# Performance work log

Hardware: AMD Instinct MI355X
Metric: run time of the kernel (lower is better)

Reference implementation:

```python
import jax, jax.numpy as jnp
import numpy as np

B, N, NODE_DIM = 64, 64, 192
H = 256          # node_hidden_dim
PDIM = 64        # property_embedding_dim
NUM_EDGE_TYPE = 5
T = 4            # message-passing rounds
E = 16384        # total edges (flattened batched graph)
E_SEL = 65536    # selected candidate pairs


def setup_inputs() -> dict:
    key = jax.random.key(0)
    ks = jax.random.split(key, 24)
    def g(k, shape, scale=0.05):
        return jax.random.normal(k, shape, dtype=jnp.float32) * scale
    inp = {
        "x": jax.random.normal(ks[0], (B, N, NODE_DIM), dtype=jnp.float32),
        "edge_index": jax.random.randint(ks[1], (2, E), 0, B * N, dtype=jnp.int32),
        "edge_attr": jax.random.uniform(ks[2], (E, NUM_EDGE_TYPE), dtype=jnp.float32),
        "props": jax.random.normal(ks[3], (B, 1), dtype=jnp.float32),
        "sel_b": jax.random.randint(ks[4], (E_SEL,), 0, B, dtype=jnp.int32),
        "sel_i": jax.random.randint(ks[5], (E_SEL,), 0, N, dtype=jnp.int32),
        "sel_j": jax.random.randint(ks[6], (E_SEL,), 0, N, dtype=jnp.int32),
        "golden_edge": jax.random.randint(ks[7], (E_SEL,), 0, NUM_EDGE_TYPE, dtype=jnp.int32),
        # parameters
        "W_prop": g(ks[8], (1, PDIM)), "b_prop": jnp.zeros((PDIM,), jnp.float32),
        "W_in": g(ks[9], (NODE_DIM, H)), "b_in": jnp.zeros((H,), jnp.float32),
        "W_msg": g(ks[10], (H + NUM_EDGE_TYPE, H)), "b_msg": jnp.zeros((H,), jnp.float32),
        "W_upd": g(ks[11], (2 * H, H)), "b_upd": jnp.zeros((H,), jnp.float32),
        "W_add": g(ks[12], (H + PDIM, H)), "b_add": jnp.zeros((H,), jnp.float32),
        "W1": g(ks[13], (2 * H, H)), "b1": jnp.zeros((H,), jnp.float32),
        "W2": g(ks[14], (H, H)), "b2": jnp.zeros((H,), jnp.float32),
        "W3": g(ks[15], (H, 2 * H)), "b3": jnp.zeros((2 * H,), jnp.float32),
        "W_out": g(ks[16], (2 * H, NUM_EDGE_TYPE)), "b_out": jnp.zeros((NUM_EDGE_TYPE,), jnp.float32),
    }
    return inp


def reference(x, edge_index, edge_attr, props, sel_b, sel_i, sel_j, golden_edge,
              W_prop, b_prop, W_in, b_in, W_msg, b_msg, W_upd, b_upd,
              W_add, b_add, W1, b1, W2, b2, W3, b3, W_out, b_out):
    BN = B * N
    node_x = x.reshape(BN, NODE_DIM)
    src, dst = edge_index[0], edge_index[1]

    # --- GNN node embedding (t rounds of message passing, opaque Encoder.embed_node) ---
    h = jax.nn.relu(node_x @ W_in + b_in)                       # [BN, H]
    for _ in range(T):
        msg_in = jnp.concatenate([h[src], edge_attr], axis=-1)  # [E, H+num_edge_type]
        msg = jax.nn.relu(msg_in @ W_msg + b_msg)               # [E, H]
        agg = jax.ops.segment_sum(msg, dst, num_segments=BN)    # [BN, H]
        h = jax.nn.relu(jnp.concatenate([h, agg], axis=-1) @ W_upd + b_upd)

    node_emb = h.reshape(B, N, H)

    # --- property conditioning + addition linear ---
    prop = props @ W_prop + b_prop                               # [B, PDIM]
    propp = jnp.broadcast_to(prop[:, None, :], (B, N, PDIM))
    node_embg = jnp.concatenate([node_emb, propp], axis=-1) @ W_add + b_add  # [B, N, H]

    # --- gather selected (src, dst) pairs directly (equiv. to repeat_interleave + boolean mask) ---
    flat = node_embg.reshape(BN, H)
    src_e = flat[sel_b * N + sel_i]                              # [E_SEL, H]
    dst_e = flat[sel_b * N + sel_j]                              # [E_SEL, H]
    pair = jnp.concatenate([src_e, dst_e], axis=-1)              # [E_SEL, 2H]

    # --- edge predictor MLP (3 layers, ReLU between) + output linear ---
    h1 = jax.nn.relu(pair @ W1 + b1)
    h2 = jax.nn.relu(h1 @ W2 + b2)
    h3 = h2 @ W3 + b3
    logits = h3 @ W_out + b_out                                  # [E_SEL, num_edge_type]

    # --- cross entropy (mean) ---
    logp = jax.nn.log_softmax(logits, axis=-1)
    loss = -jnp.mean(jnp.take_along_axis(logp, golden_edge[:, None].astype(jnp.int32), axis=-1))
    return loss
```

## Files before the change

### kernel.cpp

```cpp
#include <hip/hip_runtime.h>
#include <math.h>

#define BN 4096
#define N_PER_B 64
#define NE 16384
#define NSEL 65536
#define NET 5
#define PD 64
#define H1STR 260
#define FSTR 264
#define PTILES 4

typedef float f32x4 __attribute__((ext_vector_type(4)));
typedef float f32x16 __attribute__((ext_vector_type(16)));
typedef short short8 __attribute__((ext_vector_type(8)));
typedef short short4v __attribute__((ext_vector_type(4)));

__device__ __forceinline__ unsigned short f2bf(float f) {
    unsigned int u = __builtin_bit_cast(unsigned int, f);
    u += 0x7fff + ((u >> 16) & 1);
    return (unsigned short)(u >> 16);
}
__device__ __forceinline__ float bf_lo(unsigned int u) {
    return __builtin_bit_cast(float, u << 16);
}
__device__ __forceinline__ float bf_hi(unsigned int u) {
    return __builtin_bit_cast(float, u & 0xffff0000u);
}
__device__ __forceinline__ unsigned int pack2(float a, float b) {
    return (unsigned)f2bf(a) | ((unsigned)f2bf(b) << 16);
}
__device__ __forceinline__ short8 ld_frag(const unsigned short* p) {
    const short4v lo = *(const short4v*)(p);
    const short4v hi = *(const short4v*)(p + 4);
    return __builtin_shufflevector(lo, hi, 0, 1, 2, 3, 4, 5, 6, 7);
}
__device__ __forceinline__ unsigned int addrelu2(unsigned int a, unsigned int b, unsigned int c) {
    const float lo = fmaxf(bf_lo(a) + bf_lo(b) + bf_lo(c), 0.f);
    const float hi = fmaxf(bf_hi(a) + bf_hi(b) + bf_hi(c), 0.f);
    return pack2(lo, hi);
}

__global__ __launch_bounds__(256) void k_hist(const int* __restrict__ eidx,
                                              int* __restrict__ deg)
{
    const int e = blockIdx.x * 256 + threadIdx.x;
    atomicAdd(&deg[eidx[NE + e]], 1);
}

__global__ __launch_bounds__(256) void csr_scan(const int* __restrict__ deg,
                                                int* __restrict__ row_start,
                                                int* __restrict__ cursor)
{
    __shared__ int sums[256];
    const int tid = threadIdx.x;
    const int base = tid * 16;
    int local[16];
    int s = 0;
    #pragma unroll
    for (int i = 0; i < 16; ++i) { local[i] = s; s += deg[base + i]; }
    sums[tid] = s;
    __syncthreads();
    for (int off = 1; off < 256; off <<= 1) {
        const int v = sums[tid];
        const int add = (tid >= off) ? sums[tid - off] : 0;
        __syncthreads();
        sums[tid] = v + add;
        __syncthreads();
    }
    const int offset = (tid == 0) ? 0 : sums[tid - 1];
    #pragma unroll
    for (int i = 0; i < 16; ++i) {
        const int v = offset + local[i];
        row_start[base + i] = v;
        cursor[base + i] = v;
    }
    if (tid == 255) row_start[4096] = NE;
}

__global__ __launch_bounds__(256) void csr_scatter(const int* __restrict__ eidx,
                                                   int* __restrict__ cursor,
                                                   int* __restrict__ srcs,
                                                   int* __restrict__ epos)
{
    const int e = blockIdx.x * 256 + threadIdx.x;
    const int pos = atomicAdd(&cursor[eidx[NE + e]], 1);
    srcs[pos] = eidx[e];
    epos[e] = pos;
}

__global__ __launch_bounds__(256) void k_pre(
    const float* __restrict__ W_in, const float* __restrict__ W_msg,
    const float* __restrict__ W_upd, const float* __restrict__ W_add,
    const float* __restrict__ W1, const float* __restrict__ W2,
    const float* __restrict__ W3, const float* __restrict__ b3,
    const float* __restrict__ W_out, const float* __restrict__ b_out,
    const float* __restrict__ props, const float* __restrict__ W_prop,
    const float* __restrict__ b_prop, const float* __restrict__ b_add,
    const float* __restrict__ b_msg, const float* __restrict__ eattr,
    const int* __restrict__ epos,
    unsigned short* __restrict__ wbf, unsigned short* __restrict__ WfT,
    float* __restrict__ bfv, float* __restrict__ prop_add,
    unsigned short* __restrict__ ETc)
{
    __shared__ __align__(16) char smem[16704];
    const int blk = blockIdx.x;
    const int tid = threadIdx.x;

    if (blk < 128) {
        float (*s)[65] = (float(*)[65])smem;
        const int wsel = blk >> 4;
        const int sub = blk & 15;
        const float* src; unsigned short* dst; int K = 256;
        switch (wsel) {
            case 0: src = W_in;              dst = wbf;                         K = 192; break;
            case 1: src = W_msg;             dst = wbf + 49152;                 break;
            case 2: src = W_upd;             dst = wbf + 49152 + 65536;         break;
            case 3: src = W_upd + 256 * 256; dst = wbf + 49152 + 2 * 65536;     break;
            case 4: src = W_add;             dst = wbf + 49152 + 3 * 65536;     break;
            case 5: src = W1;                dst = wbf + 49152 + 4 * 65536;     break;
            case 6: src = W1 + 256 * 256;    dst = wbf + 49152 + 5 * 65536;     break;
            default: src = W2;               dst = wbf + 49152 + 6 * 65536;     break;
        }
        const int k0 = (sub >> 2) * 64;
        const int n0 = (sub & 3) * 64;
        if (k0 >= K) return;
        const int tn = tid & 63;
        const int tg = tid >> 6;
        #pragma unroll
        for (int i = 0; i < 16; ++i) {
            const int kk = tg * 16 + i;
            s[kk][tn] = src[(size_t)(k0 + kk) * 256 + n0 + tn];
        }
        __syncthreads();
        #pragma unroll
        for (int i = 0; i < 16; ++i) {
            const int nn = tg * 16 + i;
            dst[(size_t)(n0 + nn) * K + k0 + tn] = f2bf(s[tn][nn]);
        }
    } else if (blk < 192) {
        const int b = blk - 128;
        const float pv = props[b];
        float acc = b_add[tid];
        for (int p = 0; p < PD; ++p) {
            const float e = fmaf(pv, W_prop[p], b_prop[p]);
            acc = fmaf(e, W_add[(256 + p) * 256 + tid], acc);
        }
        prop_add[b * 256 + tid] = acc;
    } else if (blk < 449) {
        float* part = (float*)smem;
        const int cb = blk - 192;
        float acc[NET] = {0.f, 0.f, 0.f, 0.f, 0.f};
        #pragma unroll
        for (int rep = 0; rep < 2; ++rep) {
            const int j = rep * 256 + tid;
            const float wv = (cb < 256) ? W3[(size_t)cb * 512 + j] : b3[j];
            #pragma unroll
            for (int t = 0; t < NET; ++t) acc[t] = fmaf(wv, W_out[j * NET + t], acc[t]);
        }
        #pragma unroll
        for (int t = 0; t < NET; ++t)
            for (int off = 32; off >= 1; off >>= 1) acc[t] += __shfl_down(acc[t], off);
        if ((tid & 63) == 0) {
            #pragma unroll
            for (int t = 0; t < NET; ++t) part[(tid >> 6) * NET + t] = acc[t];
        }
        __syncthreads();
        if (tid == 0) {
            float s[NET];
            #pragma unroll
            for (int t = 0; t < NET; ++t)
                s[t] = part[t] + part[NET + t] + part[2 * NET + t] + part[3 * NET + t];
            if (cb < 256) {
                #pragma unroll
                for (int t = 0; t < NET; ++t) WfT[t * 256 + cb] = f2bf(s[t]);
                #pragma unroll
                for (int t = NET; t < 16; ++t) WfT[t * 256 + cb] = 0;
            } else {
                #pragma unroll
                for (int t = 0; t < NET; ++t) bfv[t] = s[t] + b_out[t];
            }
        }
    } else {
        float* ea = (float*)smem;
        int* eposs = (int*)(smem + 2560 + 64);
        const int eb = (blk - 449) * 128;
        if (tid < 160)
            *(float4*)&ea[tid * 4] = *(const float4*)(eattr + (size_t)eb * 5 + tid * 4);
        if (tid < 128) eposs[tid] = epos[eb + tid];
        __syncthreads();
        const float* Wme = W_msg + 256 * 256;
        const float w0 = Wme[0 * 256 + tid];
        const float w1 = Wme[1 * 256 + tid];
        const float w2 = Wme[2 * 256 + tid];
        const float w3 = Wme[3 * 256 + tid];
        const float w4 = Wme[4 * 256 + tid];
        const float bm = b_msg[tid];
        for (int i = 0; i < 128; ++i) {
            const float* a = ea + i * 5;
            float v = bm;
            v = fmaf(a[0], w0, v); v = fmaf(a[1], w1, v); v = fmaf(a[2], w2, v);
            v = fmaf(a[3], w3, v); v = fmaf(a[4], w4, v);
            ETc[(size_t)eposs[i] * 256 + tid] = f2bf(v);
        }
    }
}

__global__ __launch_bounds__(1024) void fstep(
    const float* __restrict__ x, const unsigned short* __restrict__ hbuf,
    const unsigned short* __restrict__ Pin, const unsigned short* __restrict__ ETc,
    const int* __restrict__ row_start, const int* __restrict__ srcs,
    const unsigned short* __restrict__ WaT, const unsigned short* __restrict__ WbT,
    const float* __restrict__ bias1,
    const unsigned short* __restrict__ Wp2T, const float* __restrict__ prop_add,
    const unsigned short* __restrict__ W1aT, const unsigned short* __restrict__ W1bT,
    unsigned short* __restrict__ hout, unsigned short* __restrict__ out1,
    unsigned short* __restrict__ out2, int mode)
{
    __shared__ __align__(16) unsigned short Hg[16 * FSTR];
    __shared__ __align__(16) unsigned short Ag[16 * FSTR];
    __shared__ __align__(16) unsigned short Hs[16 * FSTR];
    __shared__ __align__(16) unsigned short H2s[16 * FSTR];
    const int tid = threadIdx.x;
    const int w = tid >> 6;
    const int lane = tid & 63;
    const int q = lane >> 4;
    const int tx = lane & 15;
    const int m0 = blockIdx.x * 16;
    const int col = w * 16 + tx;

    if (mode != 0) {
        {
            const int r = tid >> 6;
            const int c4 = (tid & 63) * 4;
            *(uint2*)&Hg[r * FSTR + c4] =
                *(const uint2*)(hbuf + (size_t)(m0 + r) * 256 + c4);
        }
        {
            const int node = m0 + w;
            const int beg = row_start[node];
            const int end = row_start[node + 1];
            const int c = lane * 4;
            float a0 = 0.f, a1 = 0.f, a2 = 0.f, a3 = 0.f;
            for (int idx = beg; idx < end; ++idx) {
                const int src = srcs[idx];
                const uint2 pu = *(const uint2*)(Pin + (size_t)src * 256 + c);
                const uint2 eu = *(const uint2*)(ETc + (size_t)idx * 256 + c);
                a0 += fmaxf(bf_lo(pu.x) + bf_lo(eu.x), 0.f);
                a1 += fmaxf(bf_hi(pu.x) + bf_hi(eu.x), 0.f);
                a2 += fmaxf(bf_lo(pu.y) + bf_lo(eu.y), 0.f);
                a3 += fmaxf(bf_hi(pu.y) + bf_hi(eu.y), 0.f);
            }
            uint2 o; o.x = pack2(a0, a1); o.y = pack2(a2, a3);
            *(uint2*)&Ag[w * FSTR + c] = o;
        }
        __syncthreads();
    }

    f32x4 acc = (f32x4)0.f;
    if (mode == 0) {
        #pragma unroll
        for (int s = 0; s < 6; ++s) {
            const int k0 = s * 32;
            const float* ap = x + (size_t)(m0 + tx) * 192 + k0 + q * 8;
            const float4 v0 = *(const float4*)ap;
            const float4 v1 = *(const float4*)(ap + 4);
            short8 af;
            af[0] = (short)f2bf(v0.x); af[1] = (short)f2bf(v0.y);
            af[2] = (short)f2bf(v0.z); af[3] = (short)f2bf(v0.w);
            af[4] = (short)f2bf(v1.x); af[5] = (short)f2bf(v1.y);
            af[6] = (short)f2bf(v1.z); af[7] = (short)f2bf(v1.w);
            const short8 bfr = *(const short8*)(WaT + (size_t)col * 192 + k0 + q * 8);
            acc = __builtin_amdgcn_mfma_f32_16x16x32_bf16(af, bfr, acc, 0, 0, 0);
        }
    } else {
        #pragma unroll
        for (int s = 0; s < 8; ++s) {
            const int k0 = s * 32;
            const short8 af = *(const short8*)&Hg[tx * FSTR + k0 + q * 8];
            const short8 bfr = *(const short8*)(WaT + (size_t)col * 256 + k0 + q * 8);
            acc = __builtin_amdgcn_mfma_f32_16x16x32_bf16(af, bfr, acc, 0, 0, 0);
        }
        #pragma unroll
        for (int s = 0; s < 8; ++s) {
            const int k0 = s * 32;
            const short8 af = *(const short8*)&Ag[tx * FSTR + k0 + q * 8];
            const short8 bfr = *(const short8*)(WbT + (size_t)col * 256 + k0 + q * 8);
            acc = __builtin_amdgcn_mfma_f32_16x16x32_bf16(af, bfr, acc, 0, 0, 0);
        }
    }
    {
        const float bv = bias1[col];
        #pragma unroll
        for (int r = 0; r < 4; ++r) {
            const int row = q * 4 + r;
            const unsigned short us = f2bf(fmaxf(acc[r] + bv, 0.f));
            Hs[row * FSTR + col] = us;
            if (mode < 2) hout[(size_t)(m0 + row) * 256 + col] = us;
        }
    }
    __syncthreads();

    acc = (f32x4)0.f;
    #pragma unroll
    for (int s = 0; s < 8; ++s) {
        const int k0 = s * 32;
        const short8 af = *(const short8*)&Hs[tx * FSTR + k0 + q * 8];
        const short8 bfr = *(const short8*)(Wp2T + (size_t)col * 256 + k0 + q * 8);
        acc = __builtin_amdgcn_mfma_f32_16x16x32_bf16(af, bfr, acc, 0, 0, 0);
    }
    if (mode < 2) {
        #pragma unroll
        for (int r = 0; r < 4; ++r)
            out1[(size_t)(m0 + q * 4 + r) * 256 + col] = f2bf(acc[r]);
        return;
    }
    {
        const float pv = prop_add[(m0 >> 6) * 256 + col];
        #pragma unroll
        for (int r = 0; r < 4; ++r)
            H2s[(q * 4 + r) * FSTR + col] = f2bf(acc[r] + pv);
    }
    __syncthreads();

    for (int which = 0; which < 2; ++which) {
        const unsigned short* WT = which ? W1bT : W1aT;
        unsigned short* op = which ? out2 : out1;
        acc = (f32x4)0.f;
        #pragma unroll
        for (int s = 0; s < 8; ++s) {
            const int k0 = s * 32;
            const short8 af = *(const short8*)&H2s[tx * FSTR + k0 + q * 8];
            const short8 bfr = *(const short8*)(WT + (size_t)col * 256 + k0 + q * 8);
            acc = __builtin_amdgcn_mfma_f32_16x16x32_bf16(af, bfr, acc, 0, 0, 0);
        }
        #pragma unroll
        for (int r = 0; r < 4; ++r)
            op[(size_t)(m0 + q * 4 + r) * 256 + col] = f2bf(acc[r]);
    }
}

__global__ __launch_bounds__(512, 1) void pair_k(
    const unsigned short* __restrict__ A1t, const unsigned short* __restrict__ A2t,
    const float* __restrict__ b1, const unsigned short* __restrict__ W2T,
    const float* __restrict__ b2, const unsigned short* __restrict__ WfT,
    const float* __restrict__ bfv,
    const int* __restrict__ sel_b, const int* __restrict__ sel_i,
    const int* __restrict__ sel_j, const int* __restrict__ golden,
    float* __restrict__ out)
{
    __shared__ __align__(16) unsigned short sbuf[64 * H1STR];
    __shared__ __align__(16) unsigned short b1s[256];
    __shared__ float Lg[64 * 8];
    __shared__ int sidx[64 * PTILES], didx[64 * PTILES], gold[64 * PTILES];

    const int tid = threadIdx.x;
    const int w = tid >> 6;
    const int lane = tid & 63;
    const int q = lane >> 4;
    const int tx = lane & 15;
    const int m = lane & 31;
    const int hh = lane >> 5;
    const int e0 = blockIdx.x * 64 * PTILES;

    if (tid < 64 * PTILES) {
        const int e = e0 + tid;
        const int b = sel_b[e];
        sidx[tid] = b * N_PER_B + sel_i[e];
        didx[tid] = b * N_PER_B + sel_j[e];
        gold[tid] = golden[e];
    }
    if (tid < 256) b1s[tid] = f2bf(b1[tid]);

    const int pt = w & 1;
    const int cg = w >> 1;
    short8 Breg[32];
    {
        const unsigned short* bb = W2T + (size_t)(cg * 64 + m) * 256 + hh * 8;
        #pragma unroll
        for (int cc = 0; cc < 2; ++cc)
            #pragma unroll
            for (int s = 0; s < 16; ++s)
                Breg[cc * 16 + s] = *(const short8*)(bb + (size_t)cc * 32 * 256 + s * 16);
    }
    __syncthreads();

    float total = 0.f;

    for (int t = 0; t < PTILES; ++t) {
        {
            const int hw = tid >> 5;
            #pragma unroll
            for (int j = 0; j < 4; ++j) {
                const int p = j * 16 + hw;
                const unsigned short* r1 = A1t + (size_t)sidx[t * 64 + p] * 256 + m * 8;
                const unsigned short* r2 = A2t + (size_t)didx[t * 64 + p] * 256 + m * 8;
                const uint4 u1 = *(const uint4*)r1;
                const uint4 u2 = *(const uint4*)r2;
                const uint4 ub = *(const uint4*)(b1s + m * 8);
                uint2 lo2, hi2;
                lo2.x = addrelu2(u1.x, u2.x, ub.x);
                lo2.y = addrelu2(u1.y, u2.y, ub.y);
                hi2.x = addrelu2(u1.z, u2.z, ub.z);
                hi2.y = addrelu2(u1.w, u2.w, ub.w);
                unsigned short* dbase = sbuf + p * H1STR + m * 8;
                *(uint2*)(dbase) = lo2;
                *(uint2*)(dbase + 4) = hi2;
            }
        }
        __syncthreads();

        f32x16 acc0 = (f32x16)0.f;
        f32x16 acc1 = (f32x16)0.f;
        {
            const unsigned short* arow = sbuf + (size_t)(pt * 32 + m) * H1STR + hh * 8;
            #pragma unroll
            for (int s = 0; s < 16; ++s) {
                const short8 af = ld_frag(arow + s * 16);
                acc0 = __builtin_amdgcn_mfma_f32_32x32x16_bf16(af, Breg[s], acc0, 0, 0, 0);
                acc1 = __builtin_amdgcn_mfma_f32_32x32x16_bf16(af, Breg[16 + s], acc1, 0, 0, 0);
            }
        }
        __syncthreads();

        #pragma unroll
        for (int cc = 0; cc < 2; ++cc) {
            const f32x16* ap = cc ? &acc1 : &acc0;
            const int col = cg * 64 + cc * 32 + m;
            const float bv = b2[col];
            #pragma unroll
            for (int reg = 0; reg < 16; ++reg) {
                const int prow = pt * 32 + (reg & 3) + 8 * (reg >> 2) + 4 * hh;
                sbuf[prow * H1STR + col] = f2bf(fmaxf((*ap)[reg] + bv, 0.f));
            }
        }
        __syncthreads();

        if (w < 4) {
            f32x4 accL = (f32x4)0.f;
            const unsigned short* a2row = sbuf + (size_t)(w * 16 + tx) * H1STR + q * 8;
            const unsigned short* bWf = WfT + (size_t)tx * 256 + q * 8;
            #pragma unroll
            for (int s = 0; s < 8; ++s) {
                const short8 af = ld_frag(a2row + s * 32);
                const short8 bfr = *(const short8*)(bWf + s * 32);
                accL = __builtin_amdgcn_mfma_f32_16x16x32_bf16(af, bfr, accL, 0, 0, 0);
            }
            if (tx < NET) {
                const float bb = bfv[tx];
                #pragma unroll
                for (int reg = 0; reg < 4; ++reg)
                    Lg[(w * 16 + q * 4 + reg) * 8 + tx] = accL[reg] + bb;
            }
        }
        __syncthreads();

        if (tid < 64) {
            float lg[NET];
            #pragma unroll
            for (int tt = 0; tt < NET; ++tt) lg[tt] = Lg[tid * 8 + tt];
            float mx = lg[0];
            #pragma unroll
            for (int tt = 1; tt < NET; ++tt) mx = fmaxf(mx, lg[tt]);
            float s = 0.f;
            #pragma unroll
            for (int tt = 0; tt < NET; ++tt) s += expf(lg[tt] - mx);
            float ls = mx + logf(s) - lg[gold[t * 64 + tid]];
            #pragma unroll
            for (int off = 32; off >= 1; off >>= 1) ls += __shfl_xor(ls, off);
            total += ls;
        }
        __syncthreads();
    }

    if (tid == 0) atomicAdd(out, total * (1.0f / NSEL));
}

extern "C" void kernel_launch(void* const* d_in, const int* in_sizes, int n_in,
                              void* d_out, int out_size, void* d_ws, size_t ws_size,
                              hipStream_t stream) {
    (void)in_sizes; (void)n_in; (void)out_size; (void)ws_size;
    const float* x      = (const float*)d_in[0];
    const int*   eidx   = (const int*)d_in[1];
    const float* eattr  = (const float*)d_in[2];
    const float* props  = (const float*)d_in[3];
    const int*   sel_b  = (const int*)d_in[4];
    const int*   sel_i  = (const int*)d_in[5];
    const int*   sel_j  = (const int*)d_in[6];
    const int*   golden = (const int*)d_in[7];
    const float* W_prop = (const float*)d_in[8];
    const float* b_prop = (const float*)d_in[9];
    const float* W_in   = (const float*)d_in[10];
    const float* b_in   = (const float*)d_in[11];
    const float* W_msg  = (const float*)d_in[12];
    const float* b_msg  = (const float*)d_in[13];
    const float* W_upd  = (const float*)d_in[14];
    const float* b_upd  = (const float*)d_in[15];
    const float* W_add  = (const float*)d_in[16];
    const float* b_add  = (const float*)d_in[17];
    const float* W1     = (const float*)d_in[18];
    const float* b1     = (const float*)d_in[19];
    const float* W2     = (const float*)d_in[20];
    const float* b2     = (const float*)d_in[21];
    const float* W3     = (const float*)d_in[22];
    const float* b3     = (const float*)d_in[23];
    const float* W_out  = (const float*)d_in[24];
    const float* b_out  = (const float*)d_in[25];

    const size_t SEG = (size_t)BN * 256;
    unsigned short* P0   = (unsigned short*)d_ws;
    unsigned short* P1   = P0 + SEG;
    unsigned short* hA   = P1 + SEG;
    unsigned short* hB   = hA + SEG;
    unsigned short* ETc  = hB + SEG;
    unsigned short* wbf  = ETc + (size_t)NE * 256;
    unsigned short* W_inT  = wbf;
    unsigned short* WmT    = wbf + 49152;
    unsigned short* WuaT   = WmT + 65536;
    unsigned short* WubT   = WuaT + 65536;
    unsigned short* W_addT = WubT + 65536;
    unsigned short* W1aT   = W_addT + 65536;
    unsigned short* W1bT   = W1aT + 65536;
    unsigned short* W2T    = W1bT + 65536;
    unsigned short* WfT    = W2T + 65536;
    float* prop_add = (float*)(WfT + 4096);
    float* bfv = prop_add + 64 * 256;
    int* deg       = (int*)(bfv + 16);
    int* row_start = deg + 4096;
    int* cursor    = row_start + 4104;
    int* srcs      = cursor + 4096;
    int* epos      = srcs + NE;

    hipMemsetAsync(deg, 0, 4096 * sizeof(int), stream);
    k_hist<<<NE / 256, 256, 0, stream>>>(eidx, deg);
    csr_scan<<<1, 256, 0, stream>>>(deg, row_start, cursor);
    csr_scatter<<<NE / 256, 256, 0, stream>>>(eidx, cursor, srcs, epos);
    k_pre<<<577, 256, 0, stream>>>(W_in, W_msg, W_upd, W_add, W1, W2, W3, b3,
                                   W_out, b_out, props, W_prop, b_prop, b_add,
                                   b_msg, eattr, epos, wbf, WfT, bfv, prop_add, ETc);

    fstep<<<256, 1024, 0, stream>>>(x, nullptr, nullptr, ETc, row_start, srcs,
                                    W_inT, nullptr, b_in, WmT, nullptr, nullptr, nullptr,
                                    hA, P0, nullptr, 0);
    fstep<<<256, 1024, 0, stream>>>(nullptr, hA, P0, ETc, row_start, srcs,
                                    WuaT, WubT, b_upd, WmT, nullptr, nullptr, nullptr,
                                    hB, P1, nullptr, 1);
    fstep<<<256, 1024, 0, stream>>>(nullptr, hB, P1, ETc, row_start, srcs,
                                    WuaT, WubT, b_upd, WmT, nullptr, nullptr, nullptr,
                                    hA, P0, nullptr, 1);
    fstep<<<256, 1024, 0, stream>>>(nullptr, hA, P0, ETc, row_start, srcs,
                                    WuaT, WubT, b_upd, WmT, nullptr, nullptr, nullptr,
                                    hB, P1, nullptr, 1);
    fstep<<<256, 1024, 0, stream>>>(nullptr, hB, P1, ETc, row_start, srcs,
                                    WuaT, WubT, b_upd, W_addT, prop_add, W1aT, W1bT,
                                    nullptr, P0, hA, 2);

    hipMemsetAsync(d_out, 0, sizeof(float), stream);
    pair_k<<<256, 512, 0, stream>>>(P0, hA, b1, W2T, b2, WfT, bfv,
                                    sel_b, sel_i, sel_j, golden, (float*)d_out);
}
```

Measured before the change: 252.4 us.

## Fuse CSR build into one block and retune pair kernel grid and occupancy

The CSR construction goes from a memset plus three kernels (histogram, scan, scatter) to a single 1024-thread block that does the counting, scan and scatter with shared-memory atomics, removing launches and global atomics. The pair kernel handles two tiles per block instead of four, so the grid grows from 256 to 512 blocks, and launch_bounds now asks for 4 blocks per CU. The higher occupancy target can cap registers and cause spills in pair_k, and the single-block CSR runs serially on one CU.

```diff
diff --git a/kernel.cpp b/kernel.cpp
--- a/kernel.cpp
+++ b/kernel.cpp
@@ -9,7 +9,7 @@
 #define PD 64
 #define H1STR 260
 #define FSTR 264
-#define PTILES 4
+#define PTILES 2
 
 typedef float f32x4 __attribute__((ext_vector_type(4)));
 typedef float f32x16 __attribute__((ext_vector_type(16)));
@@ -41,52 +41,56 @@
     return pack2(lo, hi);
 }
 
-__global__ __launch_bounds__(256) void k_hist(const int* __restrict__ eidx,
-                                              int* __restrict__ deg)
+__global__ __launch_bounds__(1024) void csr_all(const int* __restrict__ eidx,
+                                                int* __restrict__ row_start,
+                                                int* __restrict__ srcs,
+                                                int* __restrict__ epos)
 {
-    const int e = blockIdx.x * 256 + threadIdx.x;
-    atomicAdd(&deg[eidx[NE + e]], 1);
-}
-
-__global__ __launch_bounds__(256) void csr_scan(const int* __restrict__ deg,
-                                                int* __restrict__ row_start,
-                                                int* __restrict__ cursor)
-{
-    __shared__ int sums[256];
+    __shared__ int sdeg[4096];
+    __shared__ int ssum[1024];
     const int tid = threadIdx.x;
-    const int base = tid * 16;
-    int local[16];
+
+    #pragma unroll
+    for (int i = 0; i < 4; ++i) sdeg[tid * 4 + i] = 0;
+    __syncthreads();
+
+    #pragma unroll
+    for (int i = 0; i < 16; ++i) {
+        const int e = i * 1024 + tid;
+        atomicAdd(&sdeg[eidx[NE + e]], 1);
+    }
+    __syncthreads();
+
+    int local[4];
     int s = 0;
     #pragma unroll
-    for (int i = 0; i < 16; ++i) { local[i] = s; s += deg[base + i]; }
-    sums[tid] = s;
-    __syncthreads();
-    for (int off = 1; off < 256; off <<= 1) {
-        const int v = sums[tid];
-        const int add = (tid >= off) ? sums[tid - off] : 0;
-        __syncthreads();
-        sums[tid] = v + add;
-        __syncthreads();
-    }
-    const int offset = (tid == 0) ? 0 : sums[tid - 1];
+    for (int i = 0; i < 4; ++i) { local[i] = s; s += sdeg[tid * 4 + i]; }
+    ssum[tid] = s;
+    __syncthreads();
+    for (int off = 1; off < 1024; off <<= 1) {
+        const int v = ssum[tid];
+        const int add = (tid >= off) ? ssum[tid - off] : 0;
+        __syncthreads();
+        ssum[tid] = v + add;
+        __syncthreads();
+    }
+    const int offset = (tid == 0) ? 0 : ssum[tid - 1];
+    #pragma unroll
+    for (int i = 0; i < 4; ++i) {
+        const int v = offset + local[i];
+        row_start[tid * 4 + i] = v;
+        sdeg[tid * 4 + i] = v;
+    }
+    if (tid == 1023) row_start[4096] = NE;
+    __syncthreads();
+
     #pragma unroll
     for (int i = 0; i < 16; ++i) {
-        const int v = offset + local[i];
-        row_start[base + i] = v;
-        cursor[base + i] = v;
-    }
-    if (tid == 255) row_start[4096] = NE;
-}
-
-__global__ __launch_bounds__(256) void csr_scatter(const int* __restrict__ eidx,
-                                                   int* __restrict__ cursor,
-                                                   int* __restrict__ srcs,
-                                                   int* __restrict__ epos)
-{
-    const int e = blockIdx.x * 256 + threadIdx.x;
-    const int pos = atomicAdd(&cursor[eidx[NE + e]], 1);
-    srcs[pos] = eidx[e];
-    epos[e] = pos;
+        const int e = i * 1024 + tid;
+        const int pos = atomicAdd(&sdeg[eidx[NE + e]], 1);
+        srcs[pos] = eidx[e];
+        epos[e] = pos;
+    }
 }
 
 __global__ __launch_bounds__(256) void k_pre(
@@ -340,7 +344,7 @@
     }
 }
 
-__global__ __launch_bounds__(512, 1) void pair_k(
+__global__ __launch_bounds__(512, 4) void pair_k(
     const unsigned short* __restrict__ A1t, const unsigned short* __restrict__ A2t,
     const float* __restrict__ b1, const unsigned short* __restrict__ W2T,
     const float* __restrict__ b2, const unsigned short* __restrict__ WfT,
@@ -525,16 +529,11 @@
     unsigned short* WfT    = W2T + 65536;
     float* prop_add = (float*)(WfT + 4096);
     float* bfv = prop_add + 64 * 256;
-    int* deg       = (int*)(bfv + 16);
-    int* row_start = deg + 4096;
-    int* cursor    = row_start + 4104;
-    int* srcs      = cursor + 4096;
+    int* row_start = (int*)(bfv + 16);
+    int* srcs      = row_start + 4104;
     int* epos      = srcs + NE;
 
-    hipMemsetAsync(deg, 0, 4096 * sizeof(int), stream);
-    k_hist<<<NE / 256, 256, 0, stream>>>(eidx, deg);
-    csr_scan<<<1, 256, 0, stream>>>(deg, row_start, cursor);
-    csr_scatter<<<NE / 256, 256, 0, stream>>>(eidx, cursor, srcs, epos);
+    csr_all<<<1, 1024, 0, stream>>>(eidx, row_start, srcs, epos);
     k_pre<<<577, 256, 0, stream>>>(W_in, W_msg, W_upd, W_add, W1, W2, W3, b3,
                                    W_out, b_out, props, W_prop, b_prop, b_add,
                                    b_msg, eattr, epos, wbf, WfT, bfv, prop_add, ETc);
@@ -556,6 +555,6 @@
                                     nullptr, P0, hA, 2);
 
     hipMemsetAsync(d_out, 0, sizeof(float), stream);
-    pair_k<<<256, 512, 0, stream>>>(P0, hA, b1, W2T, b2, WfT, bfv,
+    pair_k<<<NSEL / (64 * PTILES), 512, 0, stream>>>(P0, hA, b1, W2T, b2, WfT, bfv,
                                     sel_b, sel_i, sel_j, golden, (float*)d_out);
 }
```

Result: slower. 321.2 us (+27.2%).
